# Optimization experiments

Hardware: AMD Instinct MI355X
Metric: run time of the kernel (lower is better)

The kernel has to match this reference:

```python
import jax, jax.numpy as jnp
import numpy as np

DIM_IN, DIM_OUT, DIM_HID = 1024, 1024, 1024
BATCH = 16384


def setup_inputs() -> dict:
    key = jax.random.key(0)
    k1, k2, k3, k4 = jax.random.split(key, 4)
    x = jax.random.normal(k1, (BATCH, DIM_IN), dtype=jnp.float32)
    # W_slow: Linear(dim_in -> dim_out + 2*dim_hidden + 1)
    W_slow_w = jax.random.normal(k2, (DIM_OUT + 2 * DIM_HID + 1, DIM_IN), dtype=jnp.float32) * (1.0 / np.sqrt(DIM_IN))
    W_slow_b = jax.random.normal(k3, (DIM_OUT + 2 * DIM_HID + 1,), dtype=jnp.float32) * 0.01
    # W_fast: Linear(dim_hidden -> dim_out), weight initialized to zero per module
    W_fast_w = jnp.zeros((DIM_OUT, DIM_HID), dtype=jnp.float32)
    W_fast_b = jax.random.normal(k4, (DIM_OUT,), dtype=jnp.float32) * 0.01
    return {"x": x, "W_slow_w": W_slow_w, "W_slow_b": W_slow_b,
            "W_fast_w": W_fast_w, "W_fast_b": W_fast_b}


def reference(x, W_slow_w, W_slow_b, W_fast_w, W_fast_b):
    B = x.shape[0]
    s = x @ W_slow_w.T + W_slow_b                      # [B, O + 2H + 1]
    k = s[:, :DIM_HID]                                 # [B, H]
    v = s[:, DIM_HID:DIM_HID + DIM_OUT]                # [B, O]
    q = s[:, DIM_HID + DIM_OUT:DIM_HID + DIM_OUT + DIM_HID]  # [B, H]
    lr = jax.nn.sigmoid(s[:, -1:])                     # [B, 1]
    # fast-weight read with softmax key
    v_bar = jax.nn.softmax(k, axis=1) @ W_fast_w.T + W_fast_b  # [B, O]
    # delta-rule outer-product update (batched, normalized by B)
    delta = jnp.einsum('bo,bh->oh', lr * (v - v_bar), jax.nn.sigmoid(k)) / B  # [O, H]
    W_new = W_fast_w + delta
    # read with updated fast weights
    return jax.nn.softmax(q, axis=1) @ W_new.T + W_fast_b  # [B, O]
```

## Files before the change

### kernel.cpp

```cpp
#include <hip/hip_runtime.h>
#include <math.h>

static constexpr int BATCH = 16384;

typedef __attribute__((ext_vector_type(8))) __bf16 bf16x8;
typedef __attribute__((ext_vector_type(4))) float f32x4;

__device__ __forceinline__ float sigm(float x) { return 1.0f / (1.0f + expf(-x)); }

__device__ __forceinline__ unsigned short f2bf(float f) {
  unsigned u = __float_as_uint(f);
  return (unsigned short)((u + 0x7fffu + ((u >> 16) & 1u)) >> 16);
}
__device__ __forceinline__ float bf2f(unsigned short u) {
  return __uint_as_float((unsigned)u << 16);
}

template <int EPI>
__global__ __launch_bounds__(512, 2) void mgemm8(
    const unsigned short* __restrict__ Ag, const unsigned short* __restrict__ Bg,
    int lda, int ldb, const float* __restrict__ bias,
    unsigned short* __restrict__ t0, unsigned short* __restrict__ t1,
    unsigned short* __restrict__ t2, float* __restrict__ Cf,
    const unsigned short* __restrict__ vTin, const float* __restrict__ lrp,
    unsigned short* __restrict__ outT, int ldT) {
  constexpr int NT = 32;
  __shared__ unsigned short As[4 * 8192];
  __shared__ unsigned short Bs[4 * 8192];
  const int tid = threadIdx.x, lane = tid & 63, w = tid >> 6;
  const int lm = lane & 15, kg = lane >> 4;
  const int wm = w >> 2, wn = w & 3;
  const int bm = blockIdx.y * 256, bn = blockIdx.x * 256;
  const int kz = (EPI == 3) ? (blockIdx.z << 10) : 0;
  f32x4 acc[8][4] = {};

  int offA[8], offB[4];
#pragma unroll
  for (int i = 0; i < 8; i++) {
    int r = wm * 128 + i * 16 + lm;
    offA[i] = r * 32 + (((kg + r + (r >> 2)) & 3) << 3);
  }
#pragma unroll
  for (int j = 0; j < 4; j++) {
    int r = wn * 64 + j * 16 + lm;
    offB[j] = r * 32 + (((kg + r + (r >> 2)) & 3) << 3);
  }
  const unsigned short* gA[2];
  const unsigned short* gB[2];
  int ldsoff[2];
#pragma unroll
  for (int i = 0; i < 2; i++) {
    int r = i * 128 + w * 16 + (lane >> 2);
    int q = ((lane & 3) - r - (r >> 2)) & 3;
    gA[i] = Ag + (size_t)(bm + r) * lda + kz + q * 8;
    gB[i] = Bg + (size_t)(bn + r) * ldb + kz + q * 8;
    ldsoff[i] = i * 4096 + w * 512;
  }
  auto stageA = [&](int tt, int buf) {
#pragma unroll
    for (int i = 0; i < 2; i++)
      __builtin_amdgcn_global_load_lds(
          (__attribute__((address_space(1))) void*)(unsigned short*)(gA[i] + tt * 32),
          (__attribute__((address_space(3))) void*)(As + buf * 8192 + ldsoff[i]),
          16, 0, 0);
  };
  auto stageB = [&](int tt, int buf) {
#pragma unroll
    for (int i = 0; i < 2; i++)
      __builtin_amdgcn_global_load_lds(
          (__attribute__((address_space(1))) void*)(unsigned short*)(gB[i] + tt * 32),
          (__attribute__((address_space(3))) void*)(Bs + buf * 8192 + ldsoff[i]),
          16, 0, 0);
  };

  stageA(0, 0); stageB(0, 0);
  stageA(1, 1); stageB(1, 1);
  asm volatile("s_waitcnt vmcnt(4)" ::: "memory");
  __builtin_amdgcn_s_barrier();
  __builtin_amdgcn_sched_barrier(0);

  for (int t = 0; t < NT; ++t) {
    const unsigned short* Ab = As + (t & 3) * 8192;
    const unsigned short* Bb = Bs + (t & 3) * 8192;
    bf16x8 aF[4], bF[4];
#pragma unroll
    for (int i = 0; i < 4; i++) aF[i] = *(const bf16x8*)(Ab + offA[i]);
#pragma unroll
    for (int j = 0; j < 4; j++) bF[j] = *(const bf16x8*)(Bb + offB[j]);
    if (t + 2 < NT) stageA(t + 2, (t + 2) & 3);
    __builtin_amdgcn_s_barrier();
    asm volatile("s_waitcnt lgkmcnt(0)" ::: "memory");
    __builtin_amdgcn_sched_barrier(0);
    __builtin_amdgcn_s_setprio(1);
#pragma unroll
    for (int i = 0; i < 4; i++)
#pragma unroll
      for (int j = 0; j < 4; j++)
        acc[i][j] = __builtin_amdgcn_mfma_f32_16x16x32_bf16(aF[i], bF[j], acc[i][j], 0, 0, 0);
    __builtin_amdgcn_s_setprio(0);
    __builtin_amdgcn_sched_barrier(0);
    __builtin_amdgcn_s_barrier();
    bf16x8 aG[4];
#pragma unroll
    for (int i = 0; i < 4; i++) aG[i] = *(const bf16x8*)(Ab + offA[4 + i]);
    if (t + 2 < NT) stageB(t + 2, (t + 2) & 3);
    __builtin_amdgcn_s_barrier();
    asm volatile("s_waitcnt lgkmcnt(0)" ::: "memory");
    __builtin_amdgcn_sched_barrier(0);
    __builtin_amdgcn_s_setprio(1);
#pragma unroll
    for (int i = 0; i < 4; i++)
#pragma unroll
      for (int j = 0; j < 4; j++)
        acc[4 + i][j] = __builtin_amdgcn_mfma_f32_16x16x32_bf16(aG[i], bF[j], acc[4 + i][j], 0, 0, 0);
    __builtin_amdgcn_s_setprio(0);
    __builtin_amdgcn_sched_barrier(0);
    if (t < NT - 2) { asm volatile("s_waitcnt vmcnt(4)" ::: "memory"); }
    else            { asm volatile("s_waitcnt vmcnt(0)" ::: "memory"); }
    __builtin_amdgcn_s_barrier();
    __builtin_amdgcn_sched_barrier(0);
  }

#pragma unroll
  for (int i = 0; i < 8; i++) {
#pragma unroll
    for (int j = 0; j < 4; j++) {
      const int gcol = bn + wn * 64 + j * 16 + lm;
      const int grow0 = bm + wm * 128 + i * 16 + kg * 4;
      if (EPI == 0) {
        const int which = gcol >> 10;
        unsigned short* dst = which == 0 ? t0 : (which == 1 ? t1 : t2);
        const float bv = bias[gcol];
        ushort4 pk;
        pk.x = f2bf(acc[i][j][0] + bv);
        pk.y = f2bf(acc[i][j][1] + bv);
        pk.z = f2bf(acc[i][j][2] + bv);
        pk.w = f2bf(acc[i][j][3] + bv);
        *(ushort4*)(dst + (size_t)(gcol & 1023) * ldT + grow0) = pk;
      } else if (EPI == 1) {
        const float bv = bias[gcol];
        const float4 l4 = *(const float4*)(lrp + grow0);
        const ushort4 v4 = *(const ushort4*)(vTin + (size_t)gcol * ldT + grow0);
        ushort4 o;
        o.x = f2bf(l4.x * (bf2f(v4.x) - (acc[i][j][0] + bv)));
        o.y = f2bf(l4.y * (bf2f(v4.y) - (acc[i][j][1] + bv)));
        o.z = f2bf(l4.z * (bf2f(v4.z) - (acc[i][j][2] + bv)));
        o.w = f2bf(l4.w * (bf2f(v4.w) - (acc[i][j][3] + bv)));
        *(ushort4*)(outT + (size_t)gcol * ldT + grow0) = o;
      } else if (EPI == 2) {
        const float bv = bias[gcol];
#pragma unroll
        for (int r = 0; r < 4; r++)
          Cf[(size_t)(grow0 + r) * 1024 + gcol] = acc[i][j][r] + bv;
      } else {
        float* dst = Cf + (size_t)blockIdx.z * (1024ull * 1024ull);
#pragma unroll
        for (int r = 0; r < 4; r++)
          dst[(size_t)(grow0 + r) * 1024 + gcol] = acc[i][j][r];
      }
    }
  }
}

template <int EPI>
__global__ __launch_bounds__(256) void mgemm(
    const unsigned short* __restrict__ Ag, const unsigned short* __restrict__ Bg,
    int lda, int ldb, int ksl, const float* __restrict__ bias,
    unsigned short* __restrict__ t0, unsigned short* __restrict__ t1,
    unsigned short* __restrict__ t2, float* __restrict__ Cf,
    const unsigned short* __restrict__ vTin, const float* __restrict__ lrp,
    unsigned short* __restrict__ outT, int ldT) {
  __shared__ unsigned short As[128 * 32];
  __shared__ unsigned short Bs[128 * 32];
  const int tid = threadIdx.x, lane = tid & 63, w = tid >> 6;
  const int lm = lane & 15, kg = lane >> 4;
  const int mh = (w >> 1) * 64, nh = (w & 1) * 64;
  const int bm = blockIdx.y * 128, bn = blockIdx.x * 128;
  const int kstart = blockIdx.z * ksl, kend = kstart + ksl;
  f32x4 acc[4][4] = {};

  int offA[4], offB[4];
#pragma unroll
  for (int i = 0; i < 4; i++) {
    int rA = mh + i * 16 + lm;
    offA[i] = rA * 32 + (((kg + rA + (rA >> 2)) & 3) << 3);
    int rB = nh + i * 16 + lm;
    offB[i] = rB * 32 + (((kg + rB + (rB >> 2)) & 3) << 3);
  }
  int rowS[2], kcS[2];
#pragma unroll
  for (int t = 0; t < 2; t++) {
    int c = (w * 2 + t) * 64 + lane;
    rowS[t] = c >> 2;
    kcS[t] = ((((c & 3) - rowS[t] - (rowS[t] >> 2)) & 3) << 3);
  }

  for (int k0 = kstart; k0 < kend; k0 += 32) {
#pragma unroll
    for (int t = 0; t < 2; t++) {
      __builtin_amdgcn_global_load_lds(
          (__attribute__((address_space(1))) void*)(unsigned short*)(
              Ag + (size_t)(bm + rowS[t]) * lda + k0 + kcS[t]),
          (__attribute__((address_space(3))) void*)(As + (w * 2 + t) * 512), 16, 0, 0);
      __builtin_amdgcn_global_load_lds(
          (__attribute__((address_space(1))) void*)(unsigned short*)(
              Bg + (size_t)(bn + rowS[t]) * ldb + k0 + kcS[t]),
          (__attribute__((address_space(3))) void*)(Bs + (w * 2 + t) * 512), 16, 0, 0);
    }
    __syncthreads();
    bf16x8 aF[4], bF[4];
#pragma unroll
    for (int i = 0; i < 4; i++) {
      aF[i] = *(const bf16x8*)(As + offA[i]);
      bF[i] = *(const bf16x8*)(Bs + offB[i]);
    }
#pragma unroll
    for (int i = 0; i < 4; i++)
#pragma unroll
      for (int j = 0; j < 4; j++)
        acc[i][j] = __builtin_amdgcn_mfma_f32_16x16x32_bf16(aF[i], bF[j], acc[i][j], 0, 0, 0);
    __syncthreads();
  }

#pragma unroll
  for (int i = 0; i < 4; i++) {
#pragma unroll
    for (int j = 0; j < 4; j++) {
      const int gcol = bn + nh + j * 16 + lm;
      const int grow0 = bm + mh + i * 16 + kg * 4;
      if (EPI == 3) {
        float* dst = Cf + (size_t)blockIdx.z * (1024ull * 1024ull);
#pragma unroll
        for (int r = 0; r < 4; r++)
          dst[(size_t)(grow0 + r) * 1024 + gcol] = acc[i][j][r];
      }
    }
  }
}

template <bool DOSIG>
__global__ __launch_bounds__(256) void tsoftmax(
    const unsigned short* __restrict__ in, int ldin,
    unsigned short* __restrict__ rowout,
    unsigned short* __restrict__ sigT, int ldT) {
  __shared__ unsigned short tile[1024 * 16];
  __shared__ float red[16 * 17];
  const int t = threadIdx.x, bl = t & 15, fg = t >> 4;
  const int B0 = blockIdx.x * 16;
  const int f0 = fg * 64;
  float ls = 0.f;
  for (int f = f0; f < f0 + 64; f++) {
    unsigned short u = in[(size_t)f * ldin + B0 + bl];
    tile[f * 16 + bl] = u;
    ls += expf(bf2f(u));
  }
  red[bl * 17 + fg] = ls;
  __syncthreads();
  float tot = 0.f;
#pragma unroll
  for (int g = 0; g < 16; g++) tot += red[bl * 17 + g];
  const float inv = 1.0f / tot;
  for (int fb = f0; fb < f0 + 64; fb += 4) {
    float v[4];
#pragma unroll
    for (int e = 0; e < 4; e++) v[e] = bf2f(tile[(fb + e) * 16 + bl]);
    ushort4 o;
    o.x = f2bf(expf(v[0]) * inv);
    o.y = f2bf(expf(v[1]) * inv);
    o.z = f2bf(expf(v[2]) * inv);
    o.w = f2bf(expf(v[3]) * inv);
    *(ushort4*)(rowout + (size_t)(B0 + bl) * 1024 + fb) = o;
    if (DOSIG) {
#pragma unroll
      for (int e = 0; e < 4; e++)
        sigT[(size_t)(fb + e) * ldT + B0 + bl] = f2bf(sigm(v[e]));
    }
  }
}

__global__ __launch_bounds__(256) void lrx(const float* __restrict__ x,
                                           const float* __restrict__ Wsw,
                                           const float* __restrict__ Wsb,
                                           float* __restrict__ lrOut,
                                           unsigned short* __restrict__ xbf) {
  const int lane = threadIdx.x & 63, w = threadIdx.x >> 6;
  const int b = blockIdx.x * 4 + w;
  const float* xr = x + (size_t)b * 1024;
  const float* wr = Wsw + 3072ull * 1024ull;
  float sum = 0.f;
#pragma unroll
  for (int j = 0; j < 4; j++) {
    int f = lane + 64 * j;
    float4 xv = ((const float4*)xr)[f];
    float4 wv = ((const float4*)wr)[f];
    sum += xv.x * wv.x + xv.y * wv.y + xv.z * wv.z + xv.w * wv.w;
    ushort4 o = {f2bf(xv.x), f2bf(xv.y), f2bf(xv.z), f2bf(xv.w)};
    ((ushort4*)(xbf + (size_t)b * 1024))[f] = o;
  }
#pragma unroll
  for (int o = 32; o; o >>= 1) sum += __shfl_down(sum, o, 64);
  if (lane == 0) lrOut[b] = sigm(sum + Wsb[3072]);
}

__global__ __launch_bounds__(256) void cvt_bf(const float* __restrict__ in,
                                              unsigned short* __restrict__ outp) {
  size_t i = (size_t)blockIdx.x * 256 + threadIdx.x;
  float4 v = ((const float4*)in)[i];
  ushort4 o = {f2bf(v.x), f2bf(v.y), f2bf(v.z), f2bf(v.w)};
  ((ushort4*)outp)[i] = o;
}

template <int NZ>
__global__ __launch_bounds__(256) void wnewk(const float* __restrict__ P,
                                             const float* __restrict__ Wfw,
                                             unsigned short* __restrict__ wnbf) {
  const size_t i = (size_t)blockIdx.x * 256 + threadIdx.x;
  float s = 0.f;
#pragma unroll
  for (int z = 0; z < NZ; z++) s += P[(size_t)z * (1024ull * 1024ull) + i];
  wnbf[i] = f2bf(Wfw[i] + s * (1.0f / 16384.0f));
}

extern "C" void kernel_launch(void* const* d_in, const int* in_sizes, int n_in,
                              void* d_out, int out_size, void* d_ws, size_t ws_size,
                              hipStream_t stream) {
  (void)in_sizes; (void)n_in; (void)out_size;
  const float* x   = (const float*)d_in[0];
  const float* Wsw = (const float*)d_in[1];
  const float* Wsb = (const float*)d_in[2];
  const float* Wfw = (const float*)d_in[3];
  const float* Wfb = (const float*)d_in[4];
  float* out = (float*)d_out;

  const size_t MB = 1ull << 20;
  int nc;
  if      (ws_size >= 216 * MB) nc = 1;
  else if (ws_size >= 164 * MB) nc = 2;
  else if (ws_size >= 122 * MB) nc = 4;
  else                          nc = 8;
  const size_t Bc = BATCH / nc;
  const int BcI = (int)Bc;
  const int zc = 8 / nc;
  const size_t CB = Bc * 1024 * 2;

  char* p = (char*)d_ws;
  size_t off = 0;
  auto alloc = [&](size_t bytes) {
    char* cur = p + off;
    off = (off + bytes + 255) & ~(size_t)255;
    return cur;
  };
  unsigned short* wbf  = (unsigned short*)alloc(3072ull * 1024 * 2);
  unsigned short* wfbf = (unsigned short*)alloc(1024ull * 1024 * 2);
  unsigned short* wnbf = (unsigned short*)alloc(1024ull * 1024 * 2);
  float*          lr   = (float*)alloc(BATCH * 4);
  unsigned short* qsm  = (unsigned short*)alloc((size_t)BATCH * 1024 * 2);

  unsigned short *xbf, *ksm, *kt, *Ut, *vT, *qt, *SKt;
  float* P;
  if (nc == 1) {
    char* rA = alloc(CB);
    char* rB = alloc(CB);
    char* rC = alloc(CB);
    char* rD = alloc(CB);
    char* rE = alloc(CB);
    xbf = (unsigned short*)rA; ksm = (unsigned short*)rA;
    kt  = (unsigned short*)rB; Ut  = (unsigned short*)rB;
    vT  = (unsigned short*)rC;
    qt  = (unsigned short*)rD;
    P   = (float*)rC;
    SKt = (unsigned short*)rE;
  } else {
    P   = (float*)alloc(32 * MB);
    char* rA = alloc(CB);
    char* rB = alloc(CB);
    xbf = (unsigned short*)rA; ksm = (unsigned short*)rA;
    kt  = (unsigned short*)rB; Ut  = (unsigned short*)rB;
    vT  = (unsigned short*)alloc(CB);
    qt  = (unsigned short*)alloc(CB);
    SKt = (unsigned short*)alloc(CB);
  }

  cvt_bf<<<dim3(3072), 256, 0, stream>>>(Wsw, wbf);
  cvt_bf<<<dim3(1024), 256, 0, stream>>>(Wfw, wfbf);

  for (int c = 0; c < nc; c++) {
    const float* xc = x + (size_t)c * Bc * 1024;
    float* lrc = lr + (size_t)c * Bc;
    lrx<<<dim3((unsigned)(Bc / 4)), 256, 0, stream>>>(xc, Wsw, Wsb, lrc, xbf);
    mgemm8<0><<<dim3(12, (unsigned)(Bc / 256)), 512, 0, stream>>>(
        xbf, wbf, 1024, 1024, Wsb, kt, vT, qt, nullptr, nullptr, nullptr,
        nullptr, BcI);
    tsoftmax<true><<<dim3((unsigned)(Bc / 16)), 256, 0, stream>>>(
        kt, BcI, ksm, SKt, BcI);
    tsoftmax<false><<<dim3((unsigned)(Bc / 16)), 256, 0, stream>>>(
        qt, BcI, qsm + (size_t)c * Bc * 1024, nullptr, BcI);
    mgemm8<1><<<dim3(4, (unsigned)(Bc / 256)), 512, 0, stream>>>(
        ksm, wfbf, 1024, 1024, Wfb, nullptr, nullptr, nullptr, nullptr,
        vT, lrc, Ut, BcI);
    if (nc == 1) {
      mgemm8<3><<<dim3(4, 4, 16), 512, 0, stream>>>(
          Ut, SKt, BcI, BcI, nullptr, nullptr, nullptr, nullptr,
          P, nullptr, nullptr, nullptr, BcI);
    } else {
      mgemm<3><<<dim3(8, 8, zc), 256, 0, stream>>>(
          Ut, SKt, BcI, BcI, 2048, nullptr, nullptr, nullptr, nullptr,
          P + (size_t)c * zc * 1024 * 1024, nullptr, nullptr, nullptr, BcI);
    }
  }

  if (nc == 1)
    wnewk<16><<<dim3(1024 * 1024 / 256), 256, 0, stream>>>(P, Wfw, wnbf);
  else
    wnewk<8><<<dim3(1024 * 1024 / 256), 256, 0, stream>>>(P, Wfw, wnbf);

  mgemm8<2><<<dim3(4, BATCH / 256), 512, 0, stream>>>(
      qsm, wnbf, 1024, 1024, Wfb, nullptr, nullptr, nullptr, out,
      nullptr, nullptr, nullptr, 0);
}
```

Before: 504.4 us.

## Load B fragments directly from global into registers, dropping B LDS staging

Removes the shared-memory staging buffers for the B operand in the bf16 MFMA GEMM. Each wave now reads its B fragments straight from global memory into registers every k-step, and the waitcnt and barrier schedule is rearranged to match. This halves LDS usage, which may allow more resident blocks, and removes one barrier per iteration. In exchange, B loads are no longer shared between the two M-waves, are less coalesced, and their latency is only hidden within the same iteration.

```diff
diff --git a/kernel.cpp b/kernel.cpp
--- a/kernel.cpp
+++ b/kernel.cpp
@@ -26,7 +26,6 @@
     unsigned short* __restrict__ outT, int ldT) {
   constexpr int NT = 32;
   __shared__ unsigned short As[4 * 8192];
-  __shared__ unsigned short Bs[4 * 8192];
   const int tid = threadIdx.x, lane = tid & 63, w = tid >> 6;
   const int lm = lane & 15, kg = lane >> 4;
   const int wm = w >> 2, wn = w & 3;
@@ -34,26 +33,24 @@
   const int kz = (EPI == 3) ? (blockIdx.z << 10) : 0;
   f32x4 acc[8][4] = {};
 
-  int offA[8], offB[4];
+  int offA[8];
 #pragma unroll
   for (int i = 0; i < 8; i++) {
     int r = wm * 128 + i * 16 + lm;
     offA[i] = r * 32 + (((kg + r + (r >> 2)) & 3) << 3);
   }
-#pragma unroll
-  for (int j = 0; j < 4; j++) {
-    int r = wn * 64 + j * 16 + lm;
-    offB[j] = r * 32 + (((kg + r + (r >> 2)) & 3) << 3);
-  }
+  const unsigned short* gBf[4];
+#pragma unroll
+  for (int j = 0; j < 4; j++)
+    gBf[j] = Bg + (size_t)(bn + wn * 64 + j * 16 + lm) * ldb + kz + kg * 8;
+
   const unsigned short* gA[2];
-  const unsigned short* gB[2];
   int ldsoff[2];
 #pragma unroll
   for (int i = 0; i < 2; i++) {
     int r = i * 128 + w * 16 + (lane >> 2);
     int q = ((lane & 3) - r - (r >> 2)) & 3;
     gA[i] = Ag + (size_t)(bm + r) * lda + kz + q * 8;
-    gB[i] = Bg + (size_t)(bn + r) * ldb + kz + q * 8;
     ldsoff[i] = i * 4096 + w * 512;
   }
   auto stageA = [&](int tt, int buf) {
@@ -64,31 +61,25 @@
           (__attribute__((address_space(3))) void*)(As + buf * 8192 + ldsoff[i]),
           16, 0, 0);
   };
-  auto stageB = [&](int tt, int buf) {
-#pragma unroll
-    for (int i = 0; i < 2; i++)
-      __builtin_amdgcn_global_load_lds(
-          (__attribute__((address_space(1))) void*)(unsigned short*)(gB[i] + tt * 32),
-          (__attribute__((address_space(3))) void*)(Bs + buf * 8192 + ldsoff[i]),
-          16, 0, 0);
-  };
-
-  stageA(0, 0); stageB(0, 0);
-  stageA(1, 1); stageB(1, 1);
-  asm volatile("s_waitcnt vmcnt(4)" ::: "memory");
+
+  stageA(0, 0);
+  stageA(1, 1);
+  asm volatile("s_waitcnt vmcnt(2)" ::: "memory");
   __builtin_amdgcn_s_barrier();
   __builtin_amdgcn_sched_barrier(0);
 
   for (int t = 0; t < NT; ++t) {
     const unsigned short* Ab = As + (t & 3) * 8192;
-    const unsigned short* Bb = Bs + (t & 3) * 8192;
-    bf16x8 aF[4], bF[4];
+    bf16x8 bF[4];
+#pragma unroll
+    for (int j = 0; j < 4; j++) bF[j] = *(const bf16x8*)(gBf[j] + t * 32);
+    if (t + 2 < NT) stageA(t + 2, (t + 2) & 3);
+    bf16x8 aF[4];
 #pragma unroll
     for (int i = 0; i < 4; i++) aF[i] = *(const bf16x8*)(Ab + offA[i]);
-#pragma unroll
-    for (int j = 0; j < 4; j++) bF[j] = *(const bf16x8*)(Bb + offB[j]);
-    if (t + 2 < NT) stageA(t + 2, (t + 2) & 3);
     __builtin_amdgcn_s_barrier();
+    if (t < NT - 2) { asm volatile("s_waitcnt vmcnt(2)" ::: "memory"); }
+    else            { asm volatile("s_waitcnt vmcnt(0)" ::: "memory"); }
     asm volatile("s_waitcnt lgkmcnt(0)" ::: "memory");
     __builtin_amdgcn_sched_barrier(0);
     __builtin_amdgcn_s_setprio(1);
@@ -103,8 +94,6 @@
     bf16x8 aG[4];
 #pragma unroll
     for (int i = 0; i < 4; i++) aG[i] = *(const bf16x8*)(Ab + offA[4 + i]);
-    if (t + 2 < NT) stageB(t + 2, (t + 2) & 3);
-    __builtin_amdgcn_s_barrier();
     asm volatile("s_waitcnt lgkmcnt(0)" ::: "memory");
     __builtin_amdgcn_sched_barrier(0);
     __builtin_amdgcn_s_setprio(1);
@@ -115,10 +104,7 @@
         acc[4 + i][j] = __builtin_amdgcn_mfma_f32_16x16x32_bf16(aG[i], bF[j], acc[4 + i][j], 0, 0, 0);
     __builtin_amdgcn_s_setprio(0);
     __builtin_amdgcn_sched_barrier(0);
-    if (t < NT - 2) { asm volatile("s_waitcnt vmcnt(4)" ::: "memory"); }
-    else            { asm volatile("s_waitcnt vmcnt(0)" ::: "memory"); }
     __builtin_amdgcn_s_barrier();
-    __builtin_amdgcn_sched_barrier(0);
   }
 
 #pragma unroll
```

Measured after the change: 649.6 us. 1.29x slower.
